# Kernel tuning notes

Measured on AMD Instinct MI355X. Metric: run time of the kernel, lower is better.

Reference implementation:

```python
import jax, jax.numpy as jnp
import numpy as np

N_NODES = 100000


def gcn_conv(x, edge_index, W, b):
    """PyG-style GCNConv: symmetric-normalized A+I propagation of x @ W, plus bias."""
    n = x.shape[0]
    src, dst = edge_index[0], edge_index[1]
    loops = jnp.arange(n, dtype=src.dtype)
    src = jnp.concatenate([src, loops])  # add self loops
    dst = jnp.concatenate([dst, loops])
    deg = jax.ops.segment_sum(jnp.ones_like(src, dtype=x.dtype), dst, num_segments=n)
    dinv = jnp.where(deg > 0, jax.lax.rsqrt(deg), 0.0)
    norm = dinv[src] * dinv[dst]  # [E+n]
    h = x @ W  # [n, out]
    msg = h[src] * norm[:, None]  # gather + scale
    out = jax.ops.segment_sum(msg, dst, num_segments=n)  # scatter-add
    return out + b


def setup_inputs() -> dict:
    key = jax.random.key(0)
    ks = jax.random.split(key, 5)
    x = jax.random.normal(ks[0], (N_NODES, 4), dtype=jnp.float32)
    edge_index = jax.random.randint(ks[1], (2, 3200000), 0, N_NODES, dtype=jnp.int64)
    W1 = jax.random.normal(ks[2], (4, 64), dtype=jnp.float32) * 0.5
    b1 = jnp.zeros((64,), dtype=jnp.float32)
    W2 = jax.random.normal(ks[3], (64, 32), dtype=jnp.float32) * 0.125
    b2 = jnp.zeros((32,), dtype=jnp.float32)
    return {"x": x, "edge_index": edge_index, "W1": W1, "b1": b1, "W2": W2, "b2": b2}


def reference(x, edge_index, W1, b1, W2, b2):
    h = gcn_conv(x, edge_index, W1, b1)
    h = jax.nn.relu(h)
    # F.dropout with training=False is identity (eval-mode reference)
    h = gcn_conv(h, edge_index, W2, b2)
    return jnp.mean(h, axis=0)  # [32]
```

## Files before the change

### kernel.cpp

```cpp
#include <hip/hip_runtime.h>

#define ST 512
#define EPB 8192
#define CT 1024
#define FT 1024
#define S_LOG 8
#define S 256
#define CAP 8912
#define MAXB 512

__device__ __forceinline__ void gAtomAdd(float* p, float v) {
    unsafeAtomicAdd(p, v);
}

__global__ void k_init(int* __restrict__ cur_d, int* __restrict__ cur_s,
                       float* __restrict__ g, int nb) {
    int t = threadIdx.x;
    if (t < nb) { cur_d[t] = t * CAP; cur_s[t] = t * CAP; }
    if (t < 64) g[t] = 0.0f;
}

__global__ void __launch_bounds__(ST) k_sctr2(
        const int4* __restrict__ src4, const int4* __restrict__ dst4, int E,
        int* __restrict__ cur_d, int* __restrict__ cur_s,
        unsigned* __restrict__ rec_d, unsigned* __restrict__ rec_s, int nb) {
    __shared__ unsigned lrec[EPB];
    __shared__ unsigned short lbkt[EPB];
    __shared__ int cnt[MAXB];
    __shared__ int lst[MAXB];
    __shared__ int gb[MAXB];
    int t = threadIdx.x;
    int E4 = E >> 2;
    int b4 = blockIdx.x * (EPB / 4);
    int m = min(EPB, E - blockIdx.x * EPB);

    int4 dk[4], sk[4];
    bool v[4];
    #pragma unroll
    for (int k = 0; k < 4; ++k) {
        int idx = b4 + k * ST + t;
        v[k] = idx < E4;
        if (v[k]) { dk[k] = dst4[idx]; sk[k] = src4[idx]; }
    }

    for (int ph = 0; ph < 2; ++ph) {
        int* cursor = ph ? cur_s : cur_d;
        unsigned* rec = ph ? rec_s : rec_d;
        cnt[t] = 0;
        __syncthreads();
        int rk[16];
        #pragma unroll
        for (int k = 0; k < 4; ++k) {
            if (v[k]) {
                int4 K = ph ? sk[k] : dk[k];
                rk[4 * k + 0] = atomicAdd(&cnt[K.x >> S_LOG], 1);
                rk[4 * k + 1] = atomicAdd(&cnt[K.y >> S_LOG], 1);
                rk[4 * k + 2] = atomicAdd(&cnt[K.z >> S_LOG], 1);
                rk[4 * k + 3] = atomicAdd(&cnt[K.w >> S_LOG], 1);
            }
        }
        __syncthreads();
        int c = cnt[t];
        for (int o = 1; o < MAXB; o <<= 1) {
            int u = (t >= o) ? cnt[t - o] : 0;
            __syncthreads();
            cnt[t] += u;
            __syncthreads();
        }
        lst[t] = cnt[t] - c;
        gb[t] = (c > 0) ? atomicAdd(&cursor[t], c) : 0;
        __syncthreads();
        #pragma unroll
        for (int k = 0; k < 4; ++k) {
            if (v[k]) {
                int4 K = ph ? sk[k] : dk[k];
                int4 P = ph ? dk[k] : sk[k];
                int bb, p;
                bb = K.x >> S_LOG; p = lst[bb] + rk[4 * k + 0];
                lrec[p] = ((unsigned)P.x << S_LOG) | (unsigned)(K.x & (S - 1));
                lbkt[p] = (unsigned short)bb;
                bb = K.y >> S_LOG; p = lst[bb] + rk[4 * k + 1];
                lrec[p] = ((unsigned)P.y << S_LOG) | (unsigned)(K.y & (S - 1));
                lbkt[p] = (unsigned short)bb;
                bb = K.z >> S_LOG; p = lst[bb] + rk[4 * k + 2];
                lrec[p] = ((unsigned)P.z << S_LOG) | (unsigned)(K.z & (S - 1));
                lbkt[p] = (unsigned short)bb;
                bb = K.w >> S_LOG; p = lst[bb] + rk[4 * k + 3];
                lrec[p] = ((unsigned)P.w << S_LOG) | (unsigned)(K.w & (S - 1));
                lbkt[p] = (unsigned short)bb;
            }
        }
        __syncthreads();
        for (int i = t; i < m; i += ST) {
            int bb = lbkt[i];
            rec[gb[bb] + (i - lst[bb])] = lrec[i];
        }
        __syncthreads();
    }
}

__global__ void __launch_bounds__(CT) k_csry(
        unsigned* __restrict__ rec, const int* __restrict__ cur_d,
        const float4* __restrict__ x, float* __restrict__ dinv,
        float4* __restrict__ y, int* __restrict__ nst_g, int* __restrict__ nend_g,
        int n) {
    __shared__ unsigned lrec[CAP];
    __shared__ int cnt[S];
    __shared__ int nst[S];
    int b = blockIdx.x, t = threadIdx.x;
    int lo = b * CAP;
    int m = cur_d[b] - lo;
    if (t < S) cnt[t] = 0;
    __syncthreads();
    unsigned rv[9]; int rr[9];
    #pragma unroll
    for (int k = 0; k < 9; ++k) {
        int i = t + k * CT;
        if (i < m) {
            unsigned r = rec[lo + i];
            rv[k] = r;
            rr[k] = atomicAdd(&cnt[r & (S - 1)], 1);
        }
    }
    __syncthreads();
    int deg = (t < S) ? cnt[t] : 0;
    int nd = (b << S_LOG) + t;
    if (t < S && nd < n) {
        float dv = rsqrtf((float)deg + 1.0f);
        dinv[nd] = dv;
        float4 xi = x[nd];
        y[nd] = make_float4(dv * xi.x, dv * xi.y, dv * xi.z, dv * xi.w);
    }
    for (int o = 1; o < S; o <<= 1) {
        int u = (t < S && t >= o) ? cnt[t - o] : 0;
        __syncthreads();
        if (t < S) cnt[t] += u;
        __syncthreads();
    }
    if (t < S) {
        int st = cnt[t] - deg;
        nst[t] = st;
        if (nd < n) { nst_g[nd] = lo + st; nend_g[nd] = lo + st + deg; }
    }
    __syncthreads();
    #pragma unroll
    for (int k = 0; k < 9; ++k) {
        int i = t + k * CT;
        if (i < m) lrec[nst[rv[k] & (S - 1)] + rr[k]] = rv[k] >> S_LOG;
    }
    __syncthreads();
    for (int i = t; i < m; i += CT) rec[lo + i] = lrec[i];
}

__global__ void __launch_bounds__(FT) k_fuse(
        const unsigned* __restrict__ rec_d, const unsigned* __restrict__ rec_s,
        const int* __restrict__ cur_s, const int* __restrict__ nst_g,
        const int* __restrict__ nend_g, const float4* __restrict__ y,
        const float* __restrict__ dinv,
        const float* __restrict__ W1, const float* __restrict__ b1,
        float* __restrict__ g, int n) {
    __shared__ float a[S];
    __shared__ float4 lp1[S];
    __shared__ float red[FT];
    int b = blockIdx.x, t = threadIdx.x;
    if (t < S) a[t] = 0.0f;
    __syncthreads();
    int lo = b * CAP;
    int m = cur_s[b] - lo;
    int m4 = m >> 2;
    const uint4* rec4 = (const uint4*)(rec_s + lo);
    for (int i = t; i < m4; i += FT) {
        uint4 r = rec4[i];
        float d0 = dinv[r.x >> S_LOG], d1 = dinv[r.y >> S_LOG];
        float d2 = dinv[r.z >> S_LOG], d3 = dinv[r.w >> S_LOG];
        atomicAdd(&a[r.x & (S - 1)], d0);
        atomicAdd(&a[r.y & (S - 1)], d1);
        atomicAdd(&a[r.z & (S - 1)], d2);
        atomicAdd(&a[r.w & (S - 1)], d3);
    }
    for (int i = (m4 << 2) + t; i < m; i += FT) {
        unsigned r = rec_s[lo + i];
        atomicAdd(&a[r & (S - 1)], dinv[r >> S_LOG]);
    }
    int node = t >> 2, q = t & 3;
    int nd = (b << S_LOG) + node;
    if (nd < n) {
        int j1 = nend_g[nd];
        int j = nst_g[nd] + q;
        float a0 = 0.0f, a1 = 0.0f, a2 = 0.0f, a3 = 0.0f;
        for (; j + 12 < j1; j += 16) {
            int s0 = rec_d[j], s1 = rec_d[j + 4], s2 = rec_d[j + 8], s3 = rec_d[j + 12];
            float4 y0 = y[s0], y1 = y[s1], y2 = y[s2], y3 = y[s3];
            a0 += y0.x + y1.x + y2.x + y3.x;
            a1 += y0.y + y1.y + y2.y + y3.y;
            a2 += y0.z + y1.z + y2.z + y3.z;
            a3 += y0.w + y1.w + y2.w + y3.w;
        }
        for (; j < j1; j += 4) {
            float4 ys = y[rec_d[j]];
            a0 += ys.x; a1 += ys.y; a2 += ys.z; a3 += ys.w;
        }
        a0 += __shfl_down(a0, 2); a1 += __shfl_down(a1, 2);
        a2 += __shfl_down(a2, 2); a3 += __shfl_down(a3, 2);
        a0 += __shfl_down(a0, 1); a1 += __shfl_down(a1, 1);
        a2 += __shfl_down(a2, 1); a3 += __shfl_down(a3, 1);
        if (q == 0) {
            float di = dinv[nd];
            lp1[node] = make_float4(di * a0, di * a1, di * a2, di * a3);
        }
    }
    __syncthreads();
    int c = t & 63, w = t >> 6;
    float w0 = W1[c], w1 = W1[64 + c], w2 = W1[128 + c], w3 = W1[192 + c];
    float bb = b1[c];
    int nb0 = b << S_LOG;
    float facc = 0.0f;
    for (int k = w; k < S; k += 16) {
        int ndk = nb0 + k;
        if (ndk >= n) break;
        float di = dinv[ndk];
        float4 p = lp1[k];
        float4 yi = y[ndk];
        float h0 = fmaf(di, yi.x, p.x);
        float h1 = fmaf(di, yi.y, p.y);
        float h2 = fmaf(di, yi.z, p.z);
        float h3 = fmaf(di, yi.w, p.w);
        float h = fmaf(h0, w0, fmaf(h1, w1, fmaf(h2, w2, fmaf(h3, w3, bb))));
        h = fmaxf(h, 0.0f);
        float wi = fmaf(di, a[k], di * di);
        facc = fmaf(wi, h, facc);
    }
    red[t] = facc;
    __syncthreads();
    if (t < 64) {
        float s = red[t];
        #pragma unroll
        for (int o = 1; o < 16; ++o) s += red[t + 64 * o];
        gAtomAdd(&g[t], s);
    }
}

__global__ void k_final(const float* __restrict__ g, const float* __restrict__ W2,
                        const float* __restrict__ b2, float* __restrict__ out, float inv_n) {
    int j = threadIdx.x;
    if (j < 32) {
        float a = 0.0f;
        #pragma unroll
        for (int c = 0; c < 64; ++c) a = fmaf(g[c], W2[c * 32 + j], a);
        out[j] = fmaf(a, inv_n, b2[j]);
    }
}

extern "C" void kernel_launch(void* const* d_in, const int* in_sizes, int n_in,
                              void* d_out, int out_size, void* d_ws, size_t ws_size,
                              hipStream_t stream) {
    const float* x  = (const float*)d_in[0];
    const int*   ei = (const int*)d_in[1];
    const float* W1 = (const float*)d_in[2];
    const float* b1 = (const float*)d_in[3];
    const float* W2 = (const float*)d_in[4];
    const float* b2 = (const float*)d_in[5];
    float* out = (float*)d_out;

    int n = in_sizes[0] / 4;
    int E = in_sizes[1] / 2;
    const int* src = ei;
    const int* dst = ei + E;
    int NB = (n + S - 1) >> S_LOG;

    char* ws = (char*)d_ws;
    int* cur_d = (int*)ws;
    int* cur_s = cur_d + 512;
    float* g   = (float*)(cur_s + 512);
    size_t ctrl = 1600;
    unsigned* rec_d = (unsigned*)ws + ctrl;
    unsigned* rec_s = rec_d + (size_t)NB * CAP;
    float* y    = (float*)(rec_s + (size_t)NB * CAP);
    float* dinv = y + 4 * (size_t)n;
    int* nst_g  = (int*)(dinv + (size_t)n);
    int* nend_g = nst_g + (size_t)n;

    int NSB = (E + EPB - 1) / EPB;

    k_init<<<1, 512, 0, stream>>>(cur_d, cur_s, g, NB);
    k_sctr2<<<NSB, ST, 0, stream>>>((const int4*)src, (const int4*)dst, E,
                                    cur_d, cur_s, rec_d, rec_s, NB);
    k_csry<<<NB, CT, 0, stream>>>(rec_d, cur_d, (const float4*)x, dinv,
                                  (float4*)y, nst_g, nend_g, n);
    k_fuse<<<NB, FT, 0, stream>>>(rec_d, rec_s, cur_s, nst_g, nend_g,
                                  (const float4*)y, dinv, W1, b1, g, n);
    k_final<<<1, 64, 0, stream>>>(g, W2, b2, out, 1.0f / (float)n);
}
```

Baseline: 153.5 us.

## Replace per-bucket CSR build with shared-memory atomic aggregation and wave-level scan

The second kernel no longer sorts each bucket's destination records into CSR order. It only builds a degree histogram to compute dinv and the scaled features. The fused kernel then aggregates neighbor features with shared-memory float atomics per destination, reading the unsorted records directly, and the nst/nend index arrays are dropped. The scatter kernel's block-wide prefix scan is replaced by a wavefront shuffle scan plus a small per-wave sum pass, which cuts the number of barriers. This trades the sort and extra global write pass for four shared atomics per edge, which can contend, and it makes the float summation order nondeterministic.

Result: slower. 218.9 us (+42.6%).

```diff
diff --git a/kernel.cpp b/kernel.cpp
--- a/kernel.cpp
+++ b/kernel.cpp
@@ -2,7 +2,7 @@
 
 #define ST 512
 #define EPB 8192
-#define CT 1024
+#define HT 1024
 #define FT 1024
 #define S_LOG 8
 #define S 256
@@ -29,7 +29,9 @@
     __shared__ int cnt[MAXB];
     __shared__ int lst[MAXB];
     __shared__ int gb[MAXB];
+    __shared__ int wsum[8];
     int t = threadIdx.x;
+    int lane = t & 63, wv = t >> 6;
     int E4 = E >> 2;
     int b4 = blockIdx.x * (EPB / 4);
     int m = min(EPB, E - blockIdx.x * EPB);
@@ -61,13 +63,19 @@
         }
         __syncthreads();
         int c = cnt[t];
-        for (int o = 1; o < MAXB; o <<= 1) {
-            int u = (t >= o) ? cnt[t - o] : 0;
-            __syncthreads();
-            cnt[t] += u;
-            __syncthreads();
-        }
-        lst[t] = cnt[t] - c;
+        int ic = c;
+        #pragma unroll
+        for (int o = 1; o < 64; o <<= 1) {
+            int u = __shfl_up(ic, o);
+            if (lane >= o) ic += u;
+        }
+        if (lane == 63) wsum[wv] = ic;
+        __syncthreads();
+        int pre = 0;
+        #pragma unroll
+        for (int k = 0; k < 7; ++k) pre += (k < wv) ? wsum[k] : 0;
+        ic += pre;
+        lst[t] = ic - c;
         gb[t] = (c > 0) ? atomicAdd(&cursor[t], c) : 0;
         __syncthreads();
         #pragma unroll
@@ -99,78 +107,56 @@
     }
 }
 
-__global__ void __launch_bounds__(CT) k_csry(
-        unsigned* __restrict__ rec, const int* __restrict__ cur_d,
+__global__ void __launch_bounds__(HT) k_hist(
+        const unsigned* __restrict__ rec_d, const int* __restrict__ cur_d,
         const float4* __restrict__ x, float* __restrict__ dinv,
-        float4* __restrict__ y, int* __restrict__ nst_g, int* __restrict__ nend_g,
-        int n) {
-    __shared__ unsigned lrec[CAP];
+        float4* __restrict__ y, int n) {
     __shared__ int cnt[S];
-    __shared__ int nst[S];
     int b = blockIdx.x, t = threadIdx.x;
+    if (t < S) cnt[t] = 0;
+    __syncthreads();
     int lo = b * CAP;
     int m = cur_d[b] - lo;
-    if (t < S) cnt[t] = 0;
-    __syncthreads();
-    unsigned rv[9]; int rr[9];
-    #pragma unroll
-    for (int k = 0; k < 9; ++k) {
-        int i = t + k * CT;
-        if (i < m) {
-            unsigned r = rec[lo + i];
-            rv[k] = r;
-            rr[k] = atomicAdd(&cnt[r & (S - 1)], 1);
-        }
-    }
-    __syncthreads();
-    int deg = (t < S) ? cnt[t] : 0;
+    int m4 = m >> 2;
+    const uint4* rec4 = (const uint4*)(rec_d + lo);
+    for (int i = t; i < m4; i += HT) {
+        uint4 r = rec4[i];
+        atomicAdd(&cnt[r.x & (S - 1)], 1);
+        atomicAdd(&cnt[r.y & (S - 1)], 1);
+        atomicAdd(&cnt[r.z & (S - 1)], 1);
+        atomicAdd(&cnt[r.w & (S - 1)], 1);
+    }
+    for (int i = (m4 << 2) + t; i < m; i += HT)
+        atomicAdd(&cnt[rec_d[lo + i] & (S - 1)], 1);
+    __syncthreads();
     int nd = (b << S_LOG) + t;
     if (t < S && nd < n) {
-        float dv = rsqrtf((float)deg + 1.0f);
+        float dv = rsqrtf((float)cnt[t] + 1.0f);
         dinv[nd] = dv;
         float4 xi = x[nd];
         y[nd] = make_float4(dv * xi.x, dv * xi.y, dv * xi.z, dv * xi.w);
     }
-    for (int o = 1; o < S; o <<= 1) {
-        int u = (t < S && t >= o) ? cnt[t - o] : 0;
-        __syncthreads();
-        if (t < S) cnt[t] += u;
-        __syncthreads();
-    }
-    if (t < S) {
-        int st = cnt[t] - deg;
-        nst[t] = st;
-        if (nd < n) { nst_g[nd] = lo + st; nend_g[nd] = lo + st + deg; }
-    }
-    __syncthreads();
-    #pragma unroll
-    for (int k = 0; k < 9; ++k) {
-        int i = t + k * CT;
-        if (i < m) lrec[nst[rv[k] & (S - 1)] + rr[k]] = rv[k] >> S_LOG;
-    }
-    __syncthreads();
-    for (int i = t; i < m; i += CT) rec[lo + i] = lrec[i];
 }
 
 __global__ void __launch_bounds__(FT) k_fuse(
         const unsigned* __restrict__ rec_d, const unsigned* __restrict__ rec_s,
-        const int* __restrict__ cur_s, const int* __restrict__ nst_g,
-        const int* __restrict__ nend_g, const float4* __restrict__ y,
-        const float* __restrict__ dinv,
+        const int* __restrict__ cur_d, const int* __restrict__ cur_s,
+        const float4* __restrict__ y, const float* __restrict__ dinv,
         const float* __restrict__ W1, const float* __restrict__ b1,
         float* __restrict__ g, int n) {
     __shared__ float a[S];
-    __shared__ float4 lp1[S];
+    __shared__ float lp1[S][4];
     __shared__ float red[FT];
     int b = blockIdx.x, t = threadIdx.x;
     if (t < S) a[t] = 0.0f;
+    ((float*)lp1)[t] = 0.0f;
     __syncthreads();
     int lo = b * CAP;
-    int m = cur_s[b] - lo;
-    int m4 = m >> 2;
-    const uint4* rec4 = (const uint4*)(rec_s + lo);
-    for (int i = t; i < m4; i += FT) {
-        uint4 r = rec4[i];
+    int ms = cur_s[b] - lo;
+    int ms4 = ms >> 2;
+    const uint4* rs4 = (const uint4*)(rec_s + lo);
+    for (int i = t; i < ms4; i += FT) {
+        uint4 r = rs4[i];
         float d0 = dinv[r.x >> S_LOG], d1 = dinv[r.y >> S_LOG];
         float d2 = dinv[r.z >> S_LOG], d3 = dinv[r.w >> S_LOG];
         atomicAdd(&a[r.x & (S - 1)], d0);
@@ -178,36 +164,36 @@
         atomicAdd(&a[r.z & (S - 1)], d2);
         atomicAdd(&a[r.w & (S - 1)], d3);
     }
-    for (int i = (m4 << 2) + t; i < m; i += FT) {
+    for (int i = (ms4 << 2) + t; i < ms; i += FT) {
         unsigned r = rec_s[lo + i];
         atomicAdd(&a[r & (S - 1)], dinv[r >> S_LOG]);
     }
-    int node = t >> 2, q = t & 3;
-    int nd = (b << S_LOG) + node;
-    if (nd < n) {
-        int j1 = nend_g[nd];
-        int j = nst_g[nd] + q;
-        float a0 = 0.0f, a1 = 0.0f, a2 = 0.0f, a3 = 0.0f;
-        for (; j + 12 < j1; j += 16) {
-            int s0 = rec_d[j], s1 = rec_d[j + 4], s2 = rec_d[j + 8], s3 = rec_d[j + 12];
-            float4 y0 = y[s0], y1 = y[s1], y2 = y[s2], y3 = y[s3];
-            a0 += y0.x + y1.x + y2.x + y3.x;
-            a1 += y0.y + y1.y + y2.y + y3.y;
-            a2 += y0.z + y1.z + y2.z + y3.z;
-            a3 += y0.w + y1.w + y2.w + y3.w;
-        }
-        for (; j < j1; j += 4) {
-            float4 ys = y[rec_d[j]];
-            a0 += ys.x; a1 += ys.y; a2 += ys.z; a3 += ys.w;
-        }
-        a0 += __shfl_down(a0, 2); a1 += __shfl_down(a1, 2);
-        a2 += __shfl_down(a2, 2); a3 += __shfl_down(a3, 2);
-        a0 += __shfl_down(a0, 1); a1 += __shfl_down(a1, 1);
-        a2 += __shfl_down(a2, 1); a3 += __shfl_down(a3, 1);
-        if (q == 0) {
-            float di = dinv[nd];
-            lp1[node] = make_float4(di * a0, di * a1, di * a2, di * a3);
-        }
+    int md = cur_d[b] - lo;
+    int md4 = md >> 2;
+    const uint4* rd4 = (const uint4*)(rec_d + lo);
+    for (int i = t; i < md4; i += FT) {
+        uint4 r = rd4[i];
+        float4 y0 = y[r.x >> S_LOG], y1 = y[r.y >> S_LOG];
+        float4 y2 = y[r.z >> S_LOG], y3 = y[r.w >> S_LOG];
+        float* p0 = lp1[r.x & (S - 1)];
+        atomicAdd(p0 + 0, y0.x); atomicAdd(p0 + 1, y0.y);
+        atomicAdd(p0 + 2, y0.z); atomicAdd(p0 + 3, y0.w);
+        float* p1 = lp1[r.y & (S - 1)];
+        atomicAdd(p1 + 0, y1.x); atomicAdd(p1 + 1, y1.y);
+        atomicAdd(p1 + 2, y1.z); atomicAdd(p1 + 3, y1.w);
+        float* p2 = lp1[r.z & (S - 1)];
+        atomicAdd(p2 + 0, y2.x); atomicAdd(p2 + 1, y2.y);
+        atomicAdd(p2 + 2, y2.z); atomicAdd(p2 + 3, y2.w);
+        float* p3 = lp1[r.w & (S - 1)];
+        atomicAdd(p3 + 0, y3.x); atomicAdd(p3 + 1, y3.y);
+        atomicAdd(p3 + 2, y3.z); atomicAdd(p3 + 3, y3.w);
+    }
+    for (int i = (md4 << 2) + t; i < md; i += FT) {
+        unsigned r = rec_d[lo + i];
+        float4 ys = y[r >> S_LOG];
+        float* p = lp1[r & (S - 1)];
+        atomicAdd(p + 0, ys.x); atomicAdd(p + 1, ys.y);
+        atomicAdd(p + 2, ys.z); atomicAdd(p + 3, ys.w);
     }
     __syncthreads();
     int c = t & 63, w = t >> 6;
@@ -219,12 +205,11 @@
         int ndk = nb0 + k;
         if (ndk >= n) break;
         float di = dinv[ndk];
-        float4 p = lp1[k];
         float4 yi = y[ndk];
-        float h0 = fmaf(di, yi.x, p.x);
-        float h1 = fmaf(di, yi.y, p.y);
-        float h2 = fmaf(di, yi.z, p.z);
-        float h3 = fmaf(di, yi.w, p.w);
+        float h0 = di * (lp1[k][0] + yi.x);
+        float h1 = di * (lp1[k][1] + yi.y);
+        float h2 = di * (lp1[k][2] + yi.z);
+        float h3 = di * (lp1[k][3] + yi.w);
         float h = fmaf(h0, w0, fmaf(h1, w1, fmaf(h2, w2, fmaf(h3, w3, bb))));
         h = fmaxf(h, 0.0f);
         float wi = fmaf(di, a[k], di * di);
@@ -277,17 +262,15 @@
     unsigned* rec_s = rec_d + (size_t)NB * CAP;
     float* y    = (float*)(rec_s + (size_t)NB * CAP);
     float* dinv = y + 4 * (size_t)n;
-    int* nst_g  = (int*)(dinv + (size_t)n);
-    int* nend_g = nst_g + (size_t)n;
 
     int NSB = (E + EPB - 1) / EPB;
 
     k_init<<<1, 512, 0, stream>>>(cur_d, cur_s, g, NB);
     k_sctr2<<<NSB, ST, 0, stream>>>((const int4*)src, (const int4*)dst, E,
                                     cur_d, cur_s, rec_d, rec_s, NB);
-    k_csry<<<NB, CT, 0, stream>>>(rec_d, cur_d, (const float4*)x, dinv,
-                                  (float4*)y, nst_g, nend_g, n);
-    k_fuse<<<NB, FT, 0, stream>>>(rec_d, rec_s, cur_s, nst_g, nend_g,
+    k_hist<<<NB, HT, 0, stream>>>(rec_d, cur_d, (const float4*)x, dinv,
+                                  (float4*)y, n);
+    k_fuse<<<NB, FT, 0, stream>>>(rec_d, rec_s, cur_d, cur_s,
                                   (const float4*)y, dinv, W1, b1, g, n);
     k_final<<<1, 64, 0, stream>>>(g, W2, b2, out, 1.0f / (float)n);
 }
```
